# Performance work log

Hardware: AMD Instinct MI355X
Metric: run time of the kernel (lower is better)

The kernel has to match this reference:

```python
import math
import jax, jax.numpy as jnp
import numpy as np

B, S, D, H = 2, 1024, 4096, 32
HD = D // H  # 128


def _rope_freqs(seq_len, head_dim, theta=10000.0):
    inv = 1.0 / (theta ** (np.arange(0, head_dim, 2, dtype=np.float32) / head_dim))
    t = np.arange(seq_len, dtype=np.float32)
    ang = np.outer(t, inv)  # [S, HD/2]
    return jnp.asarray(np.cos(ang)), jnp.asarray(np.sin(ang))


def setup_inputs() -> dict:
    key = jax.random.key(0)
    ks = jax.random.split(key, 6)
    scale = 0.02
    x = jax.random.normal(ks[0], (B, S, D), dtype=jnp.float32)
    wq = jax.random.normal(ks[1], (D, D), dtype=jnp.float32) * scale
    wk = jax.random.normal(ks[2], (D, D), dtype=jnp.float32) * scale
    wv = jax.random.normal(ks[3], (D, D), dtype=jnp.float32) * scale
    wo = jax.random.normal(ks[4], (D, D), dtype=jnp.float32) * scale
    cache_k = jnp.zeros((B, S, H, HD), dtype=jnp.float32)
    cache_v = jnp.zeros((B, S, H, HD), dtype=jnp.float32)
    freqs_cos, freqs_sin = _rope_freqs(S, HD)
    return {"x": x, "wq": wq, "wk": wk, "wv": wv, "wo": wo,
            "cache_k": cache_k, "cache_v": cache_v,
            "freqs_cos": freqs_cos, "freqs_sin": freqs_sin, "start_pos": 0}


def _apply_rope(t, cos, sin):
    # t: [B, S, H, HD]; pairs (even, odd) along last dim form complex numbers
    t2 = t.reshape(*t.shape[:-1], HD // 2, 2)
    t0, t1 = t2[..., 0], t2[..., 1]
    c = cos[None, :, None, :]  # [1, S, 1, HD/2]
    s = sin[None, :, None, :]
    o0 = t0 * c - t1 * s
    o1 = t0 * s + t1 * c
    return jnp.stack([o0, o1], axis=-1).reshape(t.shape)


def reference(x, wq, wk, wv, wo, cache_k, cache_v, freqs_cos, freqs_sin, start_pos):
    b, s, d = x.shape
    q = (x @ wq.T).reshape(b, s, H, HD)
    k = (x @ wk.T).reshape(b, s, H, HD)  # n_kv_heads == n_heads (n_rep=1)
    v = (x @ wv.T).reshape(b, s, H, HD)
    q = _apply_rope(q, freqs_cos, freqs_sin)
    k = _apply_rope(k, freqs_cos, freqs_sin)
    # KV-cache write, then read the [0 : start_pos+s] window
    cache_k = cache_k.at[:b, start_pos:start_pos + s].set(k)
    cache_v = cache_v.at[:b, start_pos:start_pos + s].set(v)
    keys = cache_k[:b, :start_pos + s]    # [b, T, H, HD]
    values = cache_v[:b, :start_pos + s]
    scores = jnp.einsum("bqhd,bkhd->bhqk", q, keys) / math.sqrt(HD)
    attn = jax.nn.softmax(scores.astype(jnp.float32), axis=-1).astype(q.dtype)
    out = jnp.einsum("bhqk,bkhd->bqhd", attn, values).reshape(b, s, d)
    return out @ wo.T
```

## Files before the change

kernel.cpp:

```cpp
#include <hip/hip_runtime.h>

#define B_  2
#define S_  1024
#define D_  4096
#define H_  32
#define HD_ 128
#define T_  (B_*S_)

typedef short s16x8 __attribute__((ext_vector_type(8)));
typedef float f32x4 __attribute__((ext_vector_type(4)));
typedef unsigned short u16;

__device__ __forceinline__ u16 f2bf(float f) {
  unsigned int u = __float_as_uint(f);
  u += 0x7fffu + ((u >> 16) & 1u);
  return (u16)(u >> 16);
}
__device__ __forceinline__ float bf2f(u16 h) {
  return __uint_as_float(((unsigned int)h) << 16);
}
__device__ __forceinline__ void gload_lds16(const void* g, void* l) {
  __builtin_amdgcn_global_load_lds(
      (const __attribute__((address_space(1))) unsigned int*)g,
      (__attribute__((address_space(3))) unsigned int*)l, 16, 0, 0);
}
#define MFMA16(a, b, c) __builtin_amdgcn_mfma_f32_16x16x32_bf16((a), (b), (c), 0, 0, 0)

__global__ __launch_bounds__(256) void cvt_bf16(const float* __restrict__ in,
                                                u16* __restrict__ out, int n8) {
  int i = blockIdx.x * 256 + threadIdx.x;
  if (i >= n8) return;
  const float4* p = (const float4*)in + (size_t)i * 2;
  float4 a = p[0], b = p[1];
  u16 us[8] = {f2bf(a.x), f2bf(a.y), f2bf(a.z), f2bf(a.w),
               f2bf(b.x), f2bf(b.y), f2bf(b.z), f2bf(b.w)};
  *(uint4*)(out + (size_t)i * 8) = *(uint4*)us;
}

template <int NW>
__device__ __forceinline__ void stage_tile(const u16* __restrict__ g, int ldk,
                                           int row0, int k0, u16* lds,
                                           int wid, int lane) {
  const int rsub = lane >> 3;
  const int c16  = (lane & 7) ^ rsub;
#pragma unroll
  for (int l = 0; l < 16 / NW; ++l) {
    const int c = wid * (16 / NW) + l;
    gload_lds16(g + (size_t)(row0 + c * 8 + rsub) * ldk + k0 + c16 * 8,
                lds + c * 512);
  }
}

__global__ __launch_bounds__(256, 3) void gemm_qkv(const u16* __restrict__ A,
                                                   const u16* __restrict__ W,
                                                   u16* __restrict__ Oq,
                                                   u16* __restrict__ Ok,
                                                   u16* __restrict__ Ovt,
                                                   const float* __restrict__ cosb,
                                                   const float* __restrict__ sinb,
                                                   int MB, int NB, int K) {
  __shared__ __align__(16) u16 LA[128 * 64];
  __shared__ __align__(16) u16 LB[128 * 64];
  const int nwg = MB * NB;
  const int cpx = nwg >> 3;
  const int bid = blockIdx.x;
  const int swz = (bid & 7) * cpx + (bid >> 3);
  const int bm = swz / NB, bn = swz % NB;
  const int m0 = bm * 128, n0 = bn * 128;
  const int tid = threadIdx.x, wid = tid >> 6, lane = tid & 63;
  const int wr = wid >> 1, wc = wid & 1;
  const int fr = lane & 15, fq = lane >> 4;
  f32x4 acc[4][4] = {};

  for (int k0 = 0; k0 < K; k0 += 64) {
    stage_tile<4>(A, K, m0, k0, LA, wid, lane);
    stage_tile<4>(W, K, n0, k0, LB, wid, lane);
    __syncthreads();
    s16x8 bf[4][2];
#pragma unroll
    for (int ni = 0; ni < 4; ++ni)
#pragma unroll
      for (int kk = 0; kk < 2; ++kk) {
        const int rr = wc * 64 + ni * 16 + fr;
        const int s16 = (kk * 4 + fq) ^ (rr & 7);
        bf[ni][kk] = *(const s16x8*)&LB[rr * 64 + s16 * 8];
      }
#pragma unroll
    for (int mi = 0; mi < 4; ++mi) {
      const int r = wr * 64 + mi * 16 + fr;
      const s16x8 a0 = *(const s16x8*)&LA[r * 64 + ((0 + fq) ^ (r & 7)) * 8];
      const s16x8 a1 = *(const s16x8*)&LA[r * 64 + ((4 + fq) ^ (r & 7)) * 8];
#pragma unroll
      for (int ni = 0; ni < 4; ++ni)
        acc[mi][ni] = MFMA16(a0, bf[ni][0], acc[mi][ni]);
#pragma unroll
      for (int ni = 0; ni < 4; ++ni)
        acc[mi][ni] = MFMA16(a1, bf[ni][1], acc[mi][ni]);
    }
    __syncthreads();
  }

  if (n0 < 8192) {
    u16* Ob = (n0 < 4096) ? Oq : Ok;
    const int nc = n0 & 4095;
    const float sgn = (fr & 1) ? 1.f : -1.f;
#pragma unroll
    for (int mi = 0; mi < 4; ++mi)
#pragma unroll
      for (int ni = 0; ni < 4; ++ni) {
        const int col = nc + wc * 64 + ni * 16 + fr;
        const int i0 = (col & (HD_ - 1)) >> 1;
#pragma unroll
        for (int r = 0; r < 4; ++r) {
          const int row = m0 + wr * 64 + mi * 16 + fq * 4 + r;
          const int s = row & (S_ - 1);
          const float v  = acc[mi][ni][r];
          const float vo = __shfl_xor(v, 1);
          const float c  = cosb[s * (HD_ / 2) + i0];
          const float sn = sinb[s * (HD_ / 2) + i0];
          Ob[(size_t)row * 4096 + col] = f2bf(v * c + sgn * vo * sn);
        }
      }
  } else {
    const int nc = n0 - 8192;
#pragma unroll
    for (int mi = 0; mi < 4; ++mi)
#pragma unroll
      for (int ni = 0; ni < 4; ++ni) {
        const int col = nc + wc * 64 + ni * 16 + fr;
        const int h = col >> 7, d = col & (HD_ - 1);
        const int row0 = m0 + wr * 64 + mi * 16 + fq * 4;
        const int bb = row0 >> 10, s0 = row0 & (S_ - 1);
        ushort4 w;
        w.x = f2bf(acc[mi][ni][0]); w.y = f2bf(acc[mi][ni][1]);
        w.z = f2bf(acc[mi][ni][2]); w.w = f2bf(acc[mi][ni][3]);
        *(ushort4*)&Ovt[((size_t)(bb * H_ + h) * HD_ + d) * S_ + s0] = w;
      }
  }
}

__global__ __launch_bounds__(512, 2) void gemm2p_out(const u16* __restrict__ A,
                                                     const u16* __restrict__ W,
                                                     float* __restrict__ Of,
                                                     int MB, int NB, int K) {
  __shared__ __align__(16) u16 LA[2][128 * 64];
  __shared__ __align__(16) u16 LB[2][2][128 * 64];
  const int nwg = MB * NB;
  const int cpx = nwg >> 3;
  const int bid = blockIdx.x;
  const int swz = (bid & 7) * cpx + (bid >> 3);
  const int bm = swz / NB, bn = swz % NB;
  const int m0 = bm * 128, n0 = bn * 256;
  const int tid = threadIdx.x, wid = tid >> 6, lane = tid & 63;
  const int wr = wid >> 2, wc = wid & 3;
  const int fr = lane & 15, fq = lane >> 4;
  const int nkt = K >> 6;
  f32x4 acc[4][4] = {};

  auto STAGE = [&](int gidx) {
    if (gidx >= 3 * nkt) return;
    const int t = gidx / 3, part = gidx - 3 * t, slot = t & 1, k0 = t * 64;
    if (part < 2)
      stage_tile<8>(W, K, n0 + part * 128, k0, &LB[slot][part][0], wid, lane);
    else
      stage_tile<8>(A, K, m0, k0, &LA[slot][0], wid, lane);
  };

  for (int g = 0; g < 5; ++g) STAGE(g);
  asm volatile("s_waitcnt vmcnt(4)" ::: "memory");
  __builtin_amdgcn_s_barrier();

  for (int t = 0; t < nkt; ++t) {
    const int slot = t & 1;
    s16x8 af[2][2], bfr[4][2];
#pragma unroll
    for (int i = 0; i < 2; ++i)
#pragma unroll
      for (int kk = 0; kk < 2; ++kk) {
        const int r = wr * 64 + i * 16 + fr;
        const int s16 = (kk * 4 + fq) ^ (r & 7);
        af[i][kk] = *(const s16x8*)&LA[slot][r * 64 + s16 * 8];
      }
#pragma unroll
    for (int ni = 0; ni < 4; ++ni)
#pragma unroll
      for (int kk = 0; kk < 2; ++kk) {
        const int rr = (wc & 1) * 64 + ni * 16 + fr;
        const int s16 = (kk * 4 + fq) ^ (rr & 7);
        bfr[ni][kk] = *(const s16x8*)&LB[slot][wc >> 1][rr * 64 + s16 * 8];
      }
    STAGE(3 * t + 5);
    __builtin_amdgcn_s_barrier();
    __builtin_amdgcn_s_setprio(1);
#pragma unroll
    for (int kk = 0; kk < 2; ++kk)
#pragma unroll
      for (int i = 0; i < 2; ++i)
#pragma unroll
        for (int ni = 0; ni < 4; ++ni)
          acc[i][ni] = MFMA16(af[i][kk], bfr[ni][kk], acc[i][ni]);
    __builtin_amdgcn_s_setprio(0);
    __builtin_amdgcn_s_barrier();
#pragma unroll
    for (int i = 0; i < 2; ++i)
#pragma unroll
      for (int kk = 0; kk < 2; ++kk) {
        const int r = wr * 64 + (2 + i) * 16 + fr;
        const int s16 = (kk * 4 + fq) ^ (r & 7);
        af[i][kk] = *(const s16x8*)&LA[slot][r * 64 + s16 * 8];
      }
    STAGE(3 * t + 6);
    STAGE(3 * t + 7);
    if (t < nkt - 2) asm volatile("s_waitcnt vmcnt(4)" ::: "memory");
    else             asm volatile("s_waitcnt vmcnt(0)" ::: "memory");
    __builtin_amdgcn_s_barrier();
    __builtin_amdgcn_s_setprio(1);
#pragma unroll
    for (int kk = 0; kk < 2; ++kk)
#pragma unroll
      for (int i = 0; i < 2; ++i)
#pragma unroll
        for (int ni = 0; ni < 4; ++ni)
          acc[2 + i][ni] = MFMA16(af[i][kk], bfr[ni][kk], acc[2 + i][ni]);
    __builtin_amdgcn_s_setprio(0);
    __builtin_amdgcn_s_barrier();
  }

  const int Nn = NB * 256;
#pragma unroll
  for (int mi = 0; mi < 4; ++mi)
#pragma unroll
    for (int ni = 0; ni < 4; ++ni) {
      const int col = n0 + wc * 64 + ni * 16 + fr;
#pragma unroll
      for (int r = 0; r < 4; ++r) {
        const int row = m0 + wr * 64 + mi * 16 + fq * 4 + r;
        Of[(size_t)row * Nn + col] = acc[mi][ni][r];
      }
    }
}

__global__ __launch_bounds__(512) void flash_attn(const u16* __restrict__ qb,
                                                  const u16* __restrict__ kb,
                                                  const u16* __restrict__ vtb,
                                                  u16* __restrict__ ab) {
  __shared__ __align__(16) u16 Ks[64][136];
  __shared__ __align__(16) u16 Vs[128][72];
  __shared__ __align__(16) u16 Ps[8][16][72];
  const int qt = blockIdx.x, h = blockIdx.y, b = blockIdx.z;
  const int tid = threadIdx.x, wid = tid >> 6, lane = tid & 63;
  const int fr = lane & 15, fq = lane >> 4;
  const int q0 = qt * 128 + wid * 16;
  s16x8 qf[4];
  {
    size_t base = (size_t)(b * S_ + q0 + fr) * D_ + h * HD_;
#pragma unroll
    for (int kk = 0; kk < 4; ++kk) qf[kk] = *(const s16x8*)&qb[base + kk * 32 + fq * 8];
  }
  f32x4 oacc[8] = {};
  float m_i[4] = {-1e30f, -1e30f, -1e30f, -1e30f};
  float l_i[4] = {0.f, 0.f, 0.f, 0.f};
  const float sc = 0.08838834764831845f;

  for (int k0 = 0; k0 < S_; k0 += 64) {
    __syncthreads();
    for (int c = tid; c < 1024; c += 512) {
      int row = c >> 4, col = (c & 15) * 8;
      *(uint4*)&Ks[row][col] =
          *(const uint4*)&kb[(size_t)(b * S_ + k0 + row) * D_ + h * HD_ + col];
    }
    for (int c = tid; c < 1024; c += 512) {
      int row = c >> 3, col = (c & 7) * 8;
      *(uint4*)&Vs[row][col] =
          *(const uint4*)&vtb[(size_t)((b * H_ + h) * HD_ + row) * S_ + k0 + col];
    }
    __syncthreads();
    f32x4 sacc[4] = {};
    __builtin_amdgcn_s_setprio(1);
#pragma unroll
    for (int kk = 0; kk < 4; ++kk)
#pragma unroll
      for (int nb = 0; nb < 4; ++nb)
        sacc[nb] = MFMA16(qf[kk], *(const s16x8*)&Ks[nb * 16 + fr][kk * 32 + fq * 8],
                          sacc[nb]);
    __builtin_amdgcn_s_setprio(0);
#pragma unroll
    for (int r = 0; r < 4; ++r) {
      float s0 = sacc[0][r] * sc, s1 = sacc[1][r] * sc;
      float s2 = sacc[2][r] * sc, s3 = sacc[3][r] * sc;
      float mx = fmaxf(fmaxf(s0, s1), fmaxf(s2, s3));
#pragma unroll
      for (int o = 1; o < 16; o <<= 1) mx = fmaxf(mx, __shfl_xor(mx, o));
      float newm = fmaxf(m_i[r], mx);
      float fsc = __expf(m_i[r] - newm);
      m_i[r] = newm;
      float p0 = __expf(s0 - newm), p1 = __expf(s1 - newm);
      float p2 = __expf(s2 - newm), p3 = __expf(s3 - newm);
      float sum = p0 + p1 + p2 + p3;
#pragma unroll
      for (int o = 1; o < 16; o <<= 1) sum += __shfl_xor(sum, o);
      l_i[r] = l_i[r] * fsc + sum;
#pragma unroll
      for (int db = 0; db < 8; ++db) oacc[db][r] *= fsc;
      Ps[wid][fq * 4 + r][0 * 16 + fr] = f2bf(p0);
      Ps[wid][fq * 4 + r][1 * 16 + fr] = f2bf(p1);
      Ps[wid][fq * 4 + r][2 * 16 + fr] = f2bf(p2);
      Ps[wid][fq * 4 + r][3 * 16 + fr] = f2bf(p3);
    }
    s16x8 pf0 = *(const s16x8*)&Ps[wid][fr][fq * 8];
    s16x8 pf1 = *(const s16x8*)&Ps[wid][fr][32 + fq * 8];
    __builtin_amdgcn_s_setprio(1);
#pragma unroll
    for (int db = 0; db < 8; ++db)
      oacc[db] = MFMA16(pf0, *(const s16x8*)&Vs[db * 16 + fr][fq * 8], oacc[db]);
#pragma unroll
    for (int db = 0; db < 8; ++db)
      oacc[db] = MFMA16(pf1, *(const s16x8*)&Vs[db * 16 + fr][32 + fq * 8], oacc[db]);
    __builtin_amdgcn_s_setprio(0);
  }
#pragma unroll
  for (int r = 0; r < 4; ++r) {
    float inv = 1.0f / l_i[r];
    size_t rowbase = (size_t)(b * S_ + q0 + fq * 4 + r) * D_ + h * HD_;
#pragma unroll
    for (int db = 0; db < 8; ++db)
      ab[rowbase + db * 16 + fr] = f2bf(oacc[db][r] * inv);
  }
}

extern "C" void kernel_launch(void* const* d_in, const int* in_sizes, int n_in,
                              void* d_out, int out_size, void* d_ws, size_t ws_size,
                              hipStream_t stream) {
  const float* x    = (const float*)d_in[0];
  const float* wq   = (const float*)d_in[1];
  const float* wk   = (const float*)d_in[2];
  const float* wv   = (const float*)d_in[3];
  const float* wo   = (const float*)d_in[4];
  const float* fcos = (const float*)d_in[7];
  const float* fsin = (const float*)d_in[8];
  float* out = (float*)d_out;

  u16* xb  = (u16*)d_ws;
  u16* wqb = xb + (size_t)T_ * D_;
  u16* wkb = wqb + (size_t)D_ * D_;
  u16* wvb = wkb + (size_t)D_ * D_;
  u16* wob = wvb + (size_t)D_ * D_;
  u16* qb  = wob + (size_t)D_ * D_;
  u16* kb  = qb + (size_t)T_ * D_;
  u16* vb  = kb + (size_t)T_ * D_;
  u16* vtb = vb + (size_t)T_ * D_;
  u16* ab  = vtb + (size_t)T_ * D_;

  cvt_bf16<<<T_ * D_ / 8 / 256, 256, 0, stream>>>(x, xb, T_ * D_ / 8);
  cvt_bf16<<<D_ * D_ / 8 / 256, 256, 0, stream>>>(wq, wqb, D_ * D_ / 8);
  cvt_bf16<<<D_ * D_ / 8 / 256, 256, 0, stream>>>(wk, wkb, D_ * D_ / 8);
  cvt_bf16<<<D_ * D_ / 8 / 256, 256, 0, stream>>>(wv, wvb, D_ * D_ / 8);
  cvt_bf16<<<D_ * D_ / 8 / 256, 256, 0, stream>>>(wo, wob, D_ * D_ / 8);

  gemm_qkv<<<1536, 256, 0, stream>>>(xb, wqb, qb, kb, vtb, fcos, fsin, 16, 96, D_);

  flash_attn<<<dim3(S_ / 128, H_, B_), 512, 0, stream>>>(qb, kb, vtb, ab);

  gemm2p_out<<<256, 512, 0, stream>>>(ab, wob, out, 16, 16, D_);
}
```

Baseline: 484.9 us.

## Run QKV projection through pipelined double-buffered 128x256 GEMM kernel

Measured after the change: 590.8 us. +21.8%, slower.

```diff
diff --git a/kernel.cpp b/kernel.cpp
--- a/kernel.cpp
+++ b/kernel.cpp
@@ -51,98 +51,16 @@
   }
 }
 
-__global__ __launch_bounds__(256, 3) void gemm_qkv(const u16* __restrict__ A,
-                                                   const u16* __restrict__ W,
-                                                   u16* __restrict__ Oq,
-                                                   u16* __restrict__ Ok,
-                                                   u16* __restrict__ Ovt,
-                                                   const float* __restrict__ cosb,
-                                                   const float* __restrict__ sinb,
-                                                   int MB, int NB, int K) {
-  __shared__ __align__(16) u16 LA[128 * 64];
-  __shared__ __align__(16) u16 LB[128 * 64];
-  const int nwg = MB * NB;
-  const int cpx = nwg >> 3;
-  const int bid = blockIdx.x;
-  const int swz = (bid & 7) * cpx + (bid >> 3);
-  const int bm = swz / NB, bn = swz % NB;
-  const int m0 = bm * 128, n0 = bn * 128;
-  const int tid = threadIdx.x, wid = tid >> 6, lane = tid & 63;
-  const int wr = wid >> 1, wc = wid & 1;
-  const int fr = lane & 15, fq = lane >> 4;
-  f32x4 acc[4][4] = {};
-
-  for (int k0 = 0; k0 < K; k0 += 64) {
-    stage_tile<4>(A, K, m0, k0, LA, wid, lane);
-    stage_tile<4>(W, K, n0, k0, LB, wid, lane);
-    __syncthreads();
-    s16x8 bf[4][2];
-#pragma unroll
-    for (int ni = 0; ni < 4; ++ni)
-#pragma unroll
-      for (int kk = 0; kk < 2; ++kk) {
-        const int rr = wc * 64 + ni * 16 + fr;
-        const int s16 = (kk * 4 + fq) ^ (rr & 7);
-        bf[ni][kk] = *(const s16x8*)&LB[rr * 64 + s16 * 8];
-      }
-#pragma unroll
-    for (int mi = 0; mi < 4; ++mi) {
-      const int r = wr * 64 + mi * 16 + fr;
-      const s16x8 a0 = *(const s16x8*)&LA[r * 64 + ((0 + fq) ^ (r & 7)) * 8];
-      const s16x8 a1 = *(const s16x8*)&LA[r * 64 + ((4 + fq) ^ (r & 7)) * 8];
-#pragma unroll
-      for (int ni = 0; ni < 4; ++ni)
-        acc[mi][ni] = MFMA16(a0, bf[ni][0], acc[mi][ni]);
-#pragma unroll
-      for (int ni = 0; ni < 4; ++ni)
-        acc[mi][ni] = MFMA16(a1, bf[ni][1], acc[mi][ni]);
-    }
-    __syncthreads();
-  }
-
-  if (n0 < 8192) {
-    u16* Ob = (n0 < 4096) ? Oq : Ok;
-    const int nc = n0 & 4095;
-    const float sgn = (fr & 1) ? 1.f : -1.f;
-#pragma unroll
-    for (int mi = 0; mi < 4; ++mi)
-#pragma unroll
-      for (int ni = 0; ni < 4; ++ni) {
-        const int col = nc + wc * 64 + ni * 16 + fr;
-        const int i0 = (col & (HD_ - 1)) >> 1;
-#pragma unroll
-        for (int r = 0; r < 4; ++r) {
-          const int row = m0 + wr * 64 + mi * 16 + fq * 4 + r;
-          const int s = row & (S_ - 1);
-          const float v  = acc[mi][ni][r];
-          const float vo = __shfl_xor(v, 1);
-          const float c  = cosb[s * (HD_ / 2) + i0];
-          const float sn = sinb[s * (HD_ / 2) + i0];
-          Ob[(size_t)row * 4096 + col] = f2bf(v * c + sgn * vo * sn);
-        }
-      }
-  } else {
-    const int nc = n0 - 8192;
-#pragma unroll
-    for (int mi = 0; mi < 4; ++mi)
-#pragma unroll
-      for (int ni = 0; ni < 4; ++ni) {
-        const int col = nc + wc * 64 + ni * 16 + fr;
-        const int h = col >> 7, d = col & (HD_ - 1);
-        const int row0 = m0 + wr * 64 + mi * 16 + fq * 4;
-        const int bb = row0 >> 10, s0 = row0 & (S_ - 1);
-        ushort4 w;
-        w.x = f2bf(acc[mi][ni][0]); w.y = f2bf(acc[mi][ni][1]);
-        w.z = f2bf(acc[mi][ni][2]); w.w = f2bf(acc[mi][ni][3]);
-        *(ushort4*)&Ovt[((size_t)(bb * H_ + h) * HD_ + d) * S_ + s0] = w;
-      }
-  }
-}
-
-__global__ __launch_bounds__(512, 2) void gemm2p_out(const u16* __restrict__ A,
-                                                     const u16* __restrict__ W,
-                                                     float* __restrict__ Of,
-                                                     int MB, int NB, int K) {
+template <int QKV>
+__global__ __launch_bounds__(512, 2) void gemm2p(const u16* __restrict__ A,
+                                                 const u16* __restrict__ W,
+                                                 u16* __restrict__ Oq,
+                                                 u16* __restrict__ Ok,
+                                                 u16* __restrict__ Ovt,
+                                                 float* __restrict__ Of,
+                                                 const float* __restrict__ cosb,
+                                                 const float* __restrict__ sinb,
+                                                 int MB, int NB, int K) {
   __shared__ __align__(16) u16 LA[2][128 * 64];
   __shared__ __align__(16) u16 LB[2][2][128 * 64];
   const int nwg = MB * NB;
@@ -226,18 +144,58 @@
     __builtin_amdgcn_s_barrier();
   }
 
-  const int Nn = NB * 256;
-#pragma unroll
-  for (int mi = 0; mi < 4; ++mi)
-#pragma unroll
-    for (int ni = 0; ni < 4; ++ni) {
-      const int col = n0 + wc * 64 + ni * 16 + fr;
-#pragma unroll
-      for (int r = 0; r < 4; ++r) {
-        const int row = m0 + wr * 64 + mi * 16 + fq * 4 + r;
-        Of[(size_t)row * Nn + col] = acc[mi][ni][r];
+  if (QKV) {
+    if (n0 < 8192) {
+      u16* Ob = (n0 < 4096) ? Oq : Ok;
+      const int nc = n0 & 4095;
+      const float sgn = (fr & 1) ? 1.f : -1.f;
+#pragma unroll
+      for (int mi = 0; mi < 4; ++mi)
+#pragma unroll
+        for (int ni = 0; ni < 4; ++ni) {
+          const int col = nc + wc * 64 + ni * 16 + fr;
+          const int i0 = (col & (HD_ - 1)) >> 1;
+#pragma unroll
+          for (int r = 0; r < 4; ++r) {
+            const int row = m0 + wr * 64 + mi * 16 + fq * 4 + r;
+            const int s = row & (S_ - 1);
+            const float v  = acc[mi][ni][r];
+            const float vo = __shfl_xor(v, 1);
+            const float c  = cosb[s * (HD_ / 2) + i0];
+            const float sn = sinb[s * (HD_ / 2) + i0];
+            Ob[(size_t)row * 4096 + col] = f2bf(v * c + sgn * vo * sn);
+          }
+        }
+    } else {
+      const int nc = n0 - 8192;
+#pragma unroll
+      for (int mi = 0; mi < 4; ++mi)
+#pragma unroll
+        for (int ni = 0; ni < 4; ++ni) {
+          const int col = nc + wc * 64 + ni * 16 + fr;
+          const int h = col >> 7, d = col & (HD_ - 1);
+          const int row0 = m0 + wr * 64 + mi * 16 + fq * 4;
+          const int bb = row0 >> 10, s0 = row0 & (S_ - 1);
+          ushort4 w;
+          w.x = f2bf(acc[mi][ni][0]); w.y = f2bf(acc[mi][ni][1]);
+          w.z = f2bf(acc[mi][ni][2]); w.w = f2bf(acc[mi][ni][3]);
+          *(ushort4*)&Ovt[((size_t)(bb * H_ + h) * HD_ + d) * S_ + s0] = w;
+        }
+    }
+  } else {
+    const int Nn = NB * 256;
+#pragma unroll
+    for (int mi = 0; mi < 4; ++mi)
+#pragma unroll
+      for (int ni = 0; ni < 4; ++ni) {
+        const int col = n0 + wc * 64 + ni * 16 + fr;
+#pragma unroll
+        for (int r = 0; r < 4; ++r) {
+          const int row = m0 + wr * 64 + mi * 16 + fq * 4 + r;
+          Of[(size_t)row * Nn + col] = acc[mi][ni][r];
+        }
       }
-    }
+  }
 }
 
 __global__ __launch_bounds__(512) void flash_attn(const u16* __restrict__ qb,
@@ -357,9 +315,11 @@
   cvt_bf16<<<D_ * D_ / 8 / 256, 256, 0, stream>>>(wv, wvb, D_ * D_ / 8);
   cvt_bf16<<<D_ * D_ / 8 / 256, 256, 0, stream>>>(wo, wob, D_ * D_ / 8);
 
-  gemm_qkv<<<1536, 256, 0, stream>>>(xb, wqb, qb, kb, vtb, fcos, fsin, 16, 96, D_);
+  gemm2p<1><<<768, 512, 0, stream>>>(xb, wqb, qb, kb, vtb, nullptr, fcos, fsin,
+                                     16, 48, D_);
 
   flash_attn<<<dim3(S_ / 128, H_, B_), 512, 0, stream>>>(qb, kb, vtb, ab);
 
-  gemm2p_out<<<256, 512, 0, stream>>>(ab, wob, out, 16, 16, D_);
-}
+  gemm2p<0><<<256, 512, 0, stream>>>(ab, wob, nullptr, nullptr, nullptr, out,
+                                     nullptr, nullptr, 16, 16, D_);
+}
```
